# Kernel tuning notes

Measured on AMD Instinct MI355X. Metric: run time of the kernel, lower is better.

Reference implementation:

```python
import jax, jax.numpy as jnp
import numpy as np

TOPK = 3  # matches init_kwargs topk


def setup_inputs() -> dict:
    key = jax.random.key(0)
    k1, k2, k3 = jax.random.split(key, 3)
    B, N, D, E, L = 256, 1024, 1024, 8, 1000
    features = jax.random.normal(k1, (B, N, D), dtype=jnp.float32)
    gate_w = jax.random.normal(k2, (D, E), dtype=jnp.float32) * (1.0 / np.sqrt(D))
    gate_b = jnp.zeros((E,), dtype=jnp.float32)
    cls_w = jax.random.normal(k3, (E, L, D), dtype=jnp.float32) * (1.0 / np.sqrt(D))
    cls_b = jnp.zeros((E, L), dtype=jnp.float32)
    return {"features": features, "gate_w": gate_w, "gate_b": gate_b,
            "cls_w": cls_w, "cls_b": cls_b}


def reference(features, gate_w, gate_b, cls_w, cls_b):
    # features: [B, N, D]; gate_w: [D, E]; cls_w: [E, L, D]
    B = features.shape[0]
    E = cls_w.shape[0]
    gate_score = features @ gate_w + gate_b                      # [B, N, E]
    gate_prob = jax.nn.softmax(gate_score.transpose(0, 2, 1), axis=-1)  # [B, E, N] softmax over tokens
    top_v, top_i = jax.lax.top_k(gate_prob, TOPK)                # [B, E, K]
    # gather top-k token features per expert -> [B, E, K, D]
    gathered = features[jnp.arange(B)[:, None, None], top_i]
    comb_w = jax.nn.softmax(top_v, axis=-1)                      # [B, E, K]
    # per-expert linear: [B, E, K, L]
    logits = jnp.einsum('bekd,eld->bekl', gathered, cls_w) + cls_b[None, :, None, :]
    # weighted sum over K, then mean over experts -> [B, L]
    out = jnp.einsum('bekl,bek->bl', logits, comb_w) / E
    return out
```

## Files before the change

### kernel.cpp

```cpp
#include <hip/hip_runtime.h>
#include <hip/hip_bf16.h>
#include <cfloat>

#define B_ 256
#define N_ 1024
#define D_ 1024
#define E_ 8
#define L_ 1000

typedef float f32x4 __attribute__((ext_vector_type(4)));
typedef short bf16x8 __attribute__((ext_vector_type(8)));

__device__ inline unsigned short f2bf(float f) {
  unsigned u = __builtin_bit_cast(unsigned, f);
  u += 0x7fffu + ((u >> 16) & 1u);
  return (unsigned short)(u >> 16);
}

__global__ __launch_bounds__(256) void k_gate(const float* __restrict__ feat,
                                              const float* __restrict__ gate_w,
                                              float* __restrict__ scores) {
  __shared__ float gwT[E_ * D_];
  __shared__ float sm[8][132];
  const int t = threadIdx.x;
#pragma unroll
  for (int j = 0; j < 32; ++j) {
    int idx = j * 256 + t;
    int e = idx & 7, d = idx >> 3;
    gwT[e * D_ + d] = gate_w[idx];
  }
  __syncthreads();

  const int wave = t >> 6, lane = t & 63;
  const long rowBase = ((long)blockIdx.x * 4 + wave) * 8;
  const float* fbase = feat + rowBase * D_;

  float acc[64];
#pragma unroll
  for (int j = 0; j < 64; ++j) acc[j] = 0.f;

#pragma unroll
  for (int it = 0; it < 4; ++it) {
    const int d0 = it * 256 + lane * 4;
    float4 f[8];
#pragma unroll
    for (int r = 0; r < 8; ++r) f[r] = *(const float4*)(fbase + r * D_ + d0);
#pragma unroll
    for (int e = 0; e < 8; ++e) {
      const float4 g = *(const float4*)(&gwT[e * D_ + d0]);
#pragma unroll
      for (int r = 0; r < 8; ++r) {
        acc[r * 8 + e] = fmaf(f[r].x, g.x,
                         fmaf(f[r].y, g.y,
                         fmaf(f[r].z, g.z,
                         fmaf(f[r].w, g.w, acc[r * 8 + e]))));
      }
    }
  }

#pragma unroll
  for (int s = 0; s < 6; ++s) {
    const int m = 1 << s;
    const int half = 32 >> s;
    const bool up = (lane & m) != 0;
#pragma unroll
    for (int j = 0; j < half; ++j) {
      float keep = up ? acc[j + half] : acc[j];
      float send = up ? acc[j] : acc[j + half];
      float recv = __shfl_xor(send, m, 64);
      acc[j] = keep + recv;
    }
  }
  const int idx = ((lane & 1) << 5) | ((lane & 2) << 3) | ((lane & 4) << 1) |
                  ((lane & 8) >> 1) | ((lane & 16) >> 3) | ((lane & 32) >> 5);
  sm[idx & 7][wave * 8 + (idx >> 3)] = acc[0];
  __syncthreads();
  const int te = t >> 5, tr = t & 31;
  scores[(size_t)te * (B_ * N_) + (long)blockIdx.x * 32 + tr] = sm[te][tr];
}

__global__ __launch_bounds__(256) void k_topk_gather(
    const float* __restrict__ scores, const float* __restrict__ feat,
    unsigned short* __restrict__ wf) {
  __shared__ int sI[3];
  __shared__ float sC[3];
  const int t = threadIdx.x, w = t >> 6, lane = t & 63;
  const int pair = blockIdx.x;
  const int b = pair >> 3, e = pair & 7;

  if (w == 0) {
    const float* s = scores + (size_t)e * (B_ * N_) + (size_t)b * N_;
    float v[16];
#pragma unroll
    for (int j = 0; j < 4; ++j) {
      const float4 x = *(const float4*)(s + j * 256 + lane * 4);
      v[j * 4 + 0] = x.x; v[j * 4 + 1] = x.y;
      v[j * 4 + 2] = x.z; v[j * 4 + 3] = x.w;
    }

    float M[3];
    int I[3];
    float Z = 0.f;
#pragma unroll
    for (int k = 0; k < 3; ++k) {
      float lm = -FLT_MAX;
      int ln = 0x7fffffff;
#pragma unroll
      for (int j = 0; j < 4; ++j)
#pragma unroll
        for (int c = 0; c < 4; ++c) {
          const float val = v[j * 4 + c];
          if (val > lm) { lm = val; ln = j * 256 + lane * 4 + c; }
        }
#pragma unroll
      for (int s2 = 1; s2 < 64; s2 <<= 1) {
        float om = __shfl_xor(lm, s2, 64);
        int on = __shfl_xor(ln, s2, 64);
        if (om > lm || (om == lm && on < ln)) { lm = om; ln = on; }
      }
      M[k] = lm;
      I[k] = ln;
      if (k == 0) {
        float se = 0.f;
#pragma unroll
        for (int j = 0; j < 16; ++j) se += expf(v[j] - lm);
#pragma unroll
        for (int s2 = 1; s2 < 64; s2 <<= 1) se += __shfl_xor(se, s2, 64);
        Z = se;
      }
      const int slot = ln >> 8, owner = (ln >> 2) & 63, comp = ln & 3;
#pragma unroll
      for (int j = 0; j < 4; ++j)
#pragma unroll
        for (int c = 0; c < 4; ++c)
          if (j == slot && c == comp && owner == lane)
            v[j * 4 + c] = -FLT_MAX;
    }

    if (lane == 0) {
      const float p0 = 1.f / Z;
      const float p1 = expf(M[1] - M[0]) / Z;
      const float p2 = expf(M[2] - M[0]) / Z;
      const float c1 = expf(p1 - p0);
      const float c2 = expf(p2 - p0);
      const float den = 1.f + c1 + c2;
      sI[0] = I[0]; sI[1] = I[1]; sI[2] = I[2];
      sC[0] = 1.f / den; sC[1] = c1 / den; sC[2] = c2 / den;
    }
  }
  __syncthreads();

  const int i0 = sI[0], i1 = sI[1], i2 = sI[2];
  const float c0 = sC[0], c1 = sC[1], c2 = sC[2];
  const float* f = feat + (size_t)b * N_ * D_;
  const int d = t * 4;
  const float4 x = *(const float4*)(f + (size_t)i0 * D_ + d);
  const float4 y = *(const float4*)(f + (size_t)i1 * D_ + d);
  const float4 z = *(const float4*)(f + (size_t)i2 * D_ + d);
  ushort4 o;
  o.x = f2bf(c0 * x.x + c1 * y.x + c2 * z.x);
  o.y = f2bf(c0 * x.y + c1 * y.y + c2 * z.y);
  o.z = f2bf(c0 * x.z + c1 * y.z + c2 * z.z);
  o.w = f2bf(c0 * x.w + c1 * y.w + c2 * z.w);
  *(ushort4*)(wf + (size_t)pair * D_ + d) = o;
}

__global__ __launch_bounds__(512) void k_cls(const unsigned short* __restrict__ wf,
                                             const float* __restrict__ cls_w,
                                             float* __restrict__ part) {
  __shared__ uint4 Ag[2][128 * 8];
  __shared__ uint4 Bg[2][64 * 8];

  const int bx = blockIdx.x;
  const int e = bx >> 5, bt = (bx >> 4) & 1, lt = bx & 15;
  const int m0 = bt * 128, l0 = lt * 64;
  const int t = threadIdx.x;
  const int w = t >> 6, lane = t & 63;
  const int wm = w >> 1, wn = w & 1;

  const int ar = t >> 2, ag2 = t & 3;
  const int br = t >> 3, bq = t & 7;
  const int lg = (l0 + br < L_) ? (l0 + br) : (L_ - 1);
  const unsigned short* agp = wf + ((size_t)(m0 + ar) * E_ + e) * D_ + ag2 * 16;
  const float* bgp = cls_w + ((size_t)e * L_ + lg) * D_ + bq * 8;

  uint4 areg[2];
  float4 breg[2];

  auto load_regs = [&](int step) {
    const int d0 = step * 64;
    areg[0] = *(const uint4*)(agp + d0);
    areg[1] = *(const uint4*)(agp + d0 + 8);
    breg[0] = *(const float4*)(bgp + d0);
    breg[1] = *(const float4*)(bgp + d0 + 4);
  };

  auto write_lds = [&](int c) {
#pragma unroll
    for (int j = 0; j < 2; ++j)
      Ag[c][ar * 8 + ((ag2 * 2 + j) ^ (ar & 7))] = areg[j];
    uint4 p;
    p.x = (unsigned)f2bf(breg[0].x) | ((unsigned)f2bf(breg[0].y) << 16);
    p.y = (unsigned)f2bf(breg[0].z) | ((unsigned)f2bf(breg[0].w) << 16);
    p.z = (unsigned)f2bf(breg[1].x) | ((unsigned)f2bf(breg[1].y) << 16);
    p.w = (unsigned)f2bf(breg[1].z) | ((unsigned)f2bf(breg[1].w) << 16);
    Bg[c][br * 8 + (bq ^ (br & 7))] = p;
  };

  f32x4 acc[2][2];
#pragma unroll
  for (int m = 0; m < 2; ++m)
#pragma unroll
    for (int n = 0; n < 2; ++n) acc[m][n] = (f32x4){0.f, 0.f, 0.f, 0.f};

  const int l15 = lane & 15, lhi = lane >> 4;

  load_regs(0);
  for (int step = 0; step < 16; ++step) {
    const int c = step & 1;
    write_lds(c);
    if (step < 15) load_regs(step + 1);
    __syncthreads();
#pragma unroll
    for (int ks = 0; ks < 2; ++ks) {
      bf16x8 a[2], b[2];
#pragma unroll
      for (int m = 0; m < 2; ++m) {
        const int row = wm * 32 + m * 16 + l15;
        a[m] = __builtin_bit_cast(bf16x8,
                 Ag[c][row * 8 + ((ks * 4 + lhi) ^ (row & 7))]);
      }
#pragma unroll
      for (int n = 0; n < 2; ++n) {
        const int row = wn * 32 + n * 16 + l15;
        b[n] = __builtin_bit_cast(bf16x8,
                 Bg[c][row * 8 + ((ks * 4 + lhi) ^ (row & 7))]);
      }
#pragma unroll
      for (int m = 0; m < 2; ++m)
#pragma unroll
        for (int n = 0; n < 2; ++n)
          acc[m][n] = __builtin_amdgcn_mfma_f32_16x16x32_bf16(
              a[m], b[n], acc[m][n], 0, 0, 0);
    }
    __syncthreads();
  }

#pragma unroll
  for (int m = 0; m < 2; ++m) {
#pragma unroll
    for (int n = 0; n < 2; ++n) {
      const int col = l0 + wn * 32 + n * 16 + l15;
      if (col < L_) {
#pragma unroll
        for (int j = 0; j < 4; ++j) {
          const int row = m0 + wm * 32 + m * 16 + lhi * 4 + j;
          part[((size_t)e * B_ + row) * L_ + col] = acc[m][n][j];
        }
      }
    }
  }
}

__global__ __launch_bounds__(256) void k_reduce(const float* __restrict__ part,
                                                const float* __restrict__ cls_b,
                                                float* __restrict__ out) {
  const int idx = blockIdx.x * 256 + threadIdx.x;
  if (idx >= B_ * L_) return;
  const int l = idx % L_;
  float s = 0.f, bias = 0.f;
#pragma unroll
  for (int e = 0; e < 8; ++e) {
    s += part[(long)e * (B_ * L_) + idx];
    bias += cls_b[e * L_ + l];
  }
  out[idx] = (s + bias) * 0.125f;
}

extern "C" void kernel_launch(void* const* d_in, const int* in_sizes, int n_in,
                              void* d_out, int out_size, void* d_ws, size_t ws_size,
                              hipStream_t stream) {
  const float* feat   = (const float*)d_in[0];
  const float* gate_w = (const float*)d_in[1];
  const float* cls_w  = (const float*)d_in[3];
  const float* cls_b  = (const float*)d_in[4];
  float* out = (float*)d_out;

  char* ws = (char*)d_ws;
  float*          scores = (float*)ws;
  float*          part   = (float*)ws;
  unsigned short* wfb    = (unsigned short*)(ws + 8388608);

  k_gate<<<8192, 256, 0, stream>>>(feat, gate_w, scores);
  k_topk_gather<<<2048, 256, 0, stream>>>(scores, feat, wfb);
  k_cls<<<256, 512, 0, stream>>>(wfb, cls_w, part);
  k_reduce<<<1000, 256, 0, stream>>>(part, cls_b, out);
}
```

Before: 238.5 us.

## Split classifier GEMM over K halves and vectorize gate weight load

The classifier kernel now splits the D reduction into two halves, doubling the grid from 256 to 512 blocks. Each block writes its own partial slice, and the reduce kernel sums 16 partials instead of 8. The block index is reordered so that experts vary fastest, and the partial buffer moves to a separate workspace offset. The gate kernel also loads gate_w as float4 before transposing into LDS. The aim is better CU occupancy on a grid that was previously too small, at the cost of extra partial-buffer traffic in the reduce step.

```diff
diff --git a/kernel.cpp b/kernel.cpp
--- a/kernel.cpp
+++ b/kernel.cpp
@@ -23,11 +23,16 @@
   __shared__ float gwT[E_ * D_];
   __shared__ float sm[8][132];
   const int t = threadIdx.x;
-#pragma unroll
-  for (int j = 0; j < 32; ++j) {
-    int idx = j * 256 + t;
-    int e = idx & 7, d = idx >> 3;
-    gwT[e * D_ + d] = gate_w[idx];
+  const float4* gw4 = (const float4*)gate_w;
+#pragma unroll
+  for (int j = 0; j < 8; ++j) {
+    const int idx4 = j * 256 + t;
+    const float4 v = gw4[idx4];
+    const int d = idx4 >> 1, e0 = (idx4 & 1) * 4;
+    gwT[(e0 + 0) * D_ + d] = v.x;
+    gwT[(e0 + 1) * D_ + d] = v.y;
+    gwT[(e0 + 2) * D_ + d] = v.z;
+    gwT[(e0 + 3) * D_ + d] = v.w;
   }
   __syncthreads();
 
@@ -172,8 +177,8 @@
   __shared__ uint4 Bg[2][64 * 8];
 
   const int bx = blockIdx.x;
-  const int e = bx >> 5, bt = (bx >> 4) & 1, lt = bx & 15;
-  const int m0 = bt * 128, l0 = lt * 64;
+  const int e = bx & 7, kt = (bx >> 3) & 1, bt = (bx >> 4) & 1, lt = bx >> 5;
+  const int m0 = bt * 128, l0 = lt * 64, k0 = kt * 512;
   const int t = threadIdx.x;
   const int w = t >> 6, lane = t & 63;
   const int wm = w >> 1, wn = w & 1;
@@ -181,8 +186,9 @@
   const int ar = t >> 2, ag2 = t & 3;
   const int br = t >> 3, bq = t & 7;
   const int lg = (l0 + br < L_) ? (l0 + br) : (L_ - 1);
-  const unsigned short* agp = wf + ((size_t)(m0 + ar) * E_ + e) * D_ + ag2 * 16;
-  const float* bgp = cls_w + ((size_t)e * L_ + lg) * D_ + bq * 8;
+  const unsigned short* agp =
+      wf + ((size_t)(m0 + ar) * E_ + e) * D_ + k0 + ag2 * 16;
+  const float* bgp = cls_w + ((size_t)e * L_ + lg) * D_ + k0 + bq * 8;
 
   uint4 areg[2];
   float4 breg[2];
@@ -216,10 +222,10 @@
   const int l15 = lane & 15, lhi = lane >> 4;
 
   load_regs(0);
-  for (int step = 0; step < 16; ++step) {
+  for (int step = 0; step < 8; ++step) {
     const int c = step & 1;
     write_lds(c);
-    if (step < 15) load_regs(step + 1);
+    if (step < 7) load_regs(step + 1);
     __syncthreads();
 #pragma unroll
     for (int ks = 0; ks < 2; ++ks) {
@@ -255,7 +261,7 @@
 #pragma unroll
         for (int j = 0; j < 4; ++j) {
           const int row = m0 + wm * 32 + m * 16 + lhi * 4 + j;
-          part[((size_t)e * B_ + row) * L_ + col] = acc[m][n][j];
+          part[((size_t)(kt * 8 + e) * B_ + row) * L_ + col] = acc[m][n][j];
         }
       }
     }
@@ -270,10 +276,9 @@
   const int l = idx % L_;
   float s = 0.f, bias = 0.f;
 #pragma unroll
-  for (int e = 0; e < 8; ++e) {
-    s += part[(long)e * (B_ * L_) + idx];
-    bias += cls_b[e * L_ + l];
-  }
+  for (int p = 0; p < 16; ++p) s += part[(size_t)p * (B_ * L_) + idx];
+#pragma unroll
+  for (int e = 0; e < 8; ++e) bias += cls_b[e * L_ + l];
   out[idx] = (s + bias) * 0.125f;
 }
 
@@ -288,11 +293,11 @@
 
   char* ws = (char*)d_ws;
   float*          scores = (float*)ws;
-  float*          part   = (float*)ws;
   unsigned short* wfb    = (unsigned short*)(ws + 8388608);
+  float*          part   = (float*)(ws + 12582912);
 
   k_gate<<<8192, 256, 0, stream>>>(feat, gate_w, scores);
   k_topk_gather<<<2048, 256, 0, stream>>>(scores, feat, wfb);
-  k_cls<<<256, 512, 0, stream>>>(wfb, cls_w, part);
+  k_cls<<<512, 512, 0, stream>>>(wfb, cls_w, part);
   k_reduce<<<1000, 256, 0, stream>>>(part, cls_b, out);
 }
```

Measured after the change: 240.1 us. No clear change (+0.7%).
